# Optimization experiments

Measured on AMD Instinct MI355X. Metric: run time of the kernel, lower is better.

The kernel has to match this reference:

```python
import math
import jax, jax.numpy as jnp
import numpy as np

T, D, H, HD, ETA, R = 4096, 1024, 8, 64, 4, 7
EPS = 1e-5


def _discounted_sum(start_state, x, discounts):
    """state[t] = state[t-1]*discounts[t] + x[t], scanned over leading axis T."""
    def step(s, xd):
        xt, dt = xd
        s = s * dt + xt
        return s, s
    _, ys = jax.lax.scan(step, start_state, (x, discounts))
    return ys  # (T, *)


def _forward(inputs, terminations, tilde_k_prev, tilde_v_prev, s_prev, tick,
             W_kqv, b_kqv, W_p, b_p, W_proj, b_proj):
    cur_seq = inputs.shape[0]
    term = terminations.astype(inputs.dtype)

    kqv = (inputs @ W_kqv + b_kqv).reshape(cur_seq, H, 5 * HD)
    keys, queries, values, beta, gammas = jnp.split(kqv, 5, axis=-1)  # each (T,H,HD)
    p = (inputs @ W_p + b_p).reshape(cur_seq, H, 3 * ETA)
    p1, p2, p3 = jnp.split(p, 3, axis=-1)  # each (T,H,ETA)

    # feature-map expansion: outer product over (eta, head_dim) -> flatten to eta*HD
    keys = jnp.einsum('chd,chn->chnd', jax.nn.relu(keys), jax.nn.relu(p1)).reshape(cur_seq, H, ETA * HD)
    queries = jnp.einsum('chd,chn->chnd', jax.nn.relu(queries), jax.nn.relu(p2)).reshape(cur_seq, H, ETA * HD)
    gammas = jnp.einsum('chd,chn->chnd', jax.nn.sigmoid(gammas), jax.nn.sigmoid(p3)).reshape(cur_seq, H, ETA * HD)
    beta = jax.nn.sigmoid(beta)  # (T,H,HD)

    ticks = tick.reshape(1, 1) + jnp.arange(1, cur_seq + 1, dtype=inputs.dtype).reshape(-1, 1)  # (T,1)->(T,R)
    omegas = jnp.linspace(-math.pi, math.pi, R).astype(inputs.dtype).reshape(1, -1)
    occil = jnp.cos(ticks * omegas)  # (T,R)

    values = values * beta
    values = values[:, None, :, :] * occil[:, :, None, None]  # (T,R,H,HD)
    keys = keys * gammas
    s = keys  # (T,H,ETA*HD)
    keys = keys[:, None, :, :] * occil[:, :, None, None]  # (T,R,H,ETA*HD)

    not_term = (1.0 - term).reshape(cur_seq, 1, 1)
    discount_gamma = (1.0 - gammas) * not_term  # (T,H,ETA*HD)
    discount_beta = (1.0 - beta) * not_term     # (T,H,HD)

    final_keys = _discounted_sum(tilde_k_prev, keys, discount_gamma[:, None])    # (T,R,H,ETA*HD)
    final_values = _discounted_sum(tilde_v_prev, values, discount_beta[:, None])  # (T,R,H,HD)
    final_s = _discounted_sum(s_prev, s, discount_gamma)                          # (T,H,ETA*HD)

    kdq = jnp.einsum('crhd,chd->crh', final_keys, queries)
    kv = jnp.einsum('crhd,crh->chd', final_values, kdq)  # sum over r
    norm = jnp.einsum('chd,chd->ch', final_s, queries)
    attn_out = kv / (2 * R * norm[..., None] + EPS)
    attn_out = attn_out.reshape(cur_seq, H * HD) @ W_proj + b_proj  # dropout p=0.0 is identity

    new_tick = tick + cur_seq
    return attn_out, final_keys[-1], final_values[-1], final_s[-1], new_tick


def setup_inputs() -> dict:
    key = jax.random.key(0)
    ks = jax.random.split(key, 5)
    return {
        'inputs': jax.random.normal(ks[0], (T, D), jnp.float32),
        'terminations': jax.random.randint(ks[1], (T,), 0, 2, jnp.int32),
        'tilde_k_prev': jnp.zeros((R, H, ETA * HD), jnp.float32),
        'tilde_v_prev': jnp.zeros((R, H, HD), jnp.float32),
        's_prev': jnp.zeros((H, ETA * HD), jnp.float32),
        'tick': jnp.ones((1,), jnp.float32),
        'W_kqv': jax.random.normal(ks[2], (D, H * HD * 5), jnp.float32) * 0.02,
        'b_kqv': jnp.zeros((H * HD * 5,), jnp.float32),
        'W_p': jax.random.normal(ks[3], (D, H * ETA * 3), jnp.float32) * 0.02,
        'b_p': jnp.zeros((H * ETA * 3,), jnp.float32),
        'W_proj': jax.random.normal(ks[4], (H * HD, D), jnp.float32) * 0.02,
        'b_proj': jnp.zeros((D,), jnp.float32),
    }


def reference(inputs, terminations, tilde_k_prev, tilde_v_prev, s_prev, tick,
              W_kqv, b_kqv, W_p, b_p, W_proj, b_proj):
    return _forward(inputs, terminations, tilde_k_prev, tilde_v_prev, s_prev, tick,
                    W_kqv, b_kqv, W_p, b_p, W_proj, b_proj)
```

## Files before the change

kernel.cpp:

```cpp
#include <hip/hip_runtime.h>
#include <hip/hip_bf16.h>
#include <math.h>

#define T_SEQ 4096
#define DIM   1024
#define NH    8
#define HDIM  64
#define ETA   4
#define NR    7
#define NKQVC 2688
#define CHUNK 16
#define NCHUNK 256

typedef __attribute__((ext_vector_type(8))) short bf16x8;
typedef __attribute__((ext_vector_type(4))) short short4v;
typedef __attribute__((ext_vector_type(4))) float f32x4;

#define KQVC_OFF    0ul
#define OCC_OFF     5505024ul
#define BTPROJ_OFF  5537792ul
#define ATTNBF_OFF  5799936ul
#define BIASC_OFF   6848512ul
#define ABF_OFF     6851328ul
#define BTCAT_OFF   8948480ul
#define YSUM_OFF    6851328ul

#define O_ATTN 0ul
#define O_FK   4194304ul
#define O_FV   4208640ul
#define O_FS   4212224ul
#define O_TICK 4214272ul

__device__ __forceinline__ float sigm(float x) { return 1.f / (1.f + __expf(-x)); }

__device__ __forceinline__ short f2bf(float f) {
  union { __hip_bfloat16 b; short s; } u;
  u.b = __float2bfloat16(f);
  return u.s;
}
__device__ __forceinline__ float bf2f(short s) {
  union { __hip_bfloat16 b; short s2; } u;
  u.s2 = s;
  return __bfloat162float(u.b);
}

__device__ __forceinline__ void gload16(const void* g, void* l) {
  __builtin_amdgcn_global_load_lds(
      (const __attribute__((address_space(1))) void*)g,
      (__attribute__((address_space(3))) void*)l, 16, 0, 0);
}

__global__ __launch_bounds__(256) void cast_f32_bf16(
    const float* __restrict__ x, short* __restrict__ y) {
  size_t i = (size_t)(blockIdx.x * 256 + threadIdx.x) * 4;
  float4 v = *(const float4*)(x + i);
  short4v o;
  o.x = f2bf(v.x); o.y = f2bf(v.y); o.z = f2bf(v.z); o.w = f2bf(v.w);
  *(short4v*)(y + i) = o;
}

__global__ __launch_bounds__(256) void transpose_cast(
    const float* __restrict__ W, short* __restrict__ Bt, int K, int N) {
  __shared__ float tile[32][33];
  int n0 = blockIdx.x * 32, k0 = blockIdx.y * 32;
  int tx = threadIdx.x, ty = threadIdx.y;
  for (int i = ty; i < 32; i += 8)
    tile[i][tx] = W[(size_t)(k0 + i) * N + n0 + tx];
  __syncthreads();
  for (int i = ty; i < 32; i += 8)
    Bt[(size_t)(n0 + i) * K + k0 + tx] = f2bf(tile[tx][i]);
}

__global__ __launch_bounds__(256) void concat_bias(
    const float* __restrict__ b_kqv, const float* __restrict__ b_p,
    float* __restrict__ bc) {
  int i = blockIdx.x * 256 + threadIdx.x;
  if (i >= NKQVC) return;
  bc[i] = (i < 2560) ? b_kqv[i] : (i < 2656 ? b_p[i - 2560] : 0.f);
}

template <int OUT_BF16>
__global__ __launch_bounds__(256) void gemm_bt_mfma(
    const short* __restrict__ A, const short* __restrict__ Bt,
    const float* __restrict__ bias, void* __restrict__ Cout,
    int M, int N, int K) {
  __shared__ __align__(16) short lds[16384];

  int nwg = gridDim.x;
  int cpx = nwg >> 3;
  int bid = blockIdx.x;
  int swz = (bid & 7) * cpx + (bid >> 3);
  int nbx = N >> 7;
  int bm0 = (swz / nbx) << 7;
  int bn0 = (swz % nbx) << 7;

  const int tid = threadIdx.x;
  const int w = tid >> 6, l = tid & 63;
  const int wm = w >> 1, wn = w & 1;
  const int fr = l & 15;
  const int fq = l >> 4;

  const int ca = w * 2;
  const short* Ag0 = A + (size_t)(bm0 + ca * 16 + (l >> 2)) * K + (l & 3) * 8;
  const short* Ag1 = Ag0 + (size_t)16 * K;
  const short* Bg0 = Bt + (size_t)(bn0 + ca * 16 + (l >> 2)) * K + (l & 3) * 8;
  const short* Bg1 = Bg0 + (size_t)16 * K;

  f32x4 acc[4][4];
#pragma unroll
  for (int mi = 0; mi < 4; ++mi)
#pragma unroll
    for (int ni = 0; ni < 4; ++ni)
#pragma unroll
      for (int r = 0; r < 4; ++r) acc[mi][ni][r] = 0.f;

  const int KT = K >> 5;
  int cur = 0;
  {
    short* la = &lds[ca * 512];
    short* lb = &lds[4096 + ca * 512];
    gload16(Ag0, la);
    gload16(Ag1, la + 512);
    gload16(Bg0, lb);
    gload16(Bg1, lb + 512);
  }
  __syncthreads();

  for (int kt = 0; kt < KT; ++kt) {
    if (kt + 1 < KT) {
      int nb = (cur ^ 1) * 8192;
      int ko = (kt + 1) * 32;
      short* la = &lds[nb + ca * 512];
      short* lb = &lds[nb + 4096 + ca * 512];
      gload16(Ag0 + ko, la);
      gload16(Ag1 + ko, la + 512);
      gload16(Bg0 + ko, lb);
      gload16(Bg1 + ko, lb + 512);
    }
    const short* ArP = &lds[cur * 8192 + (wm * 64 + fr) * 32 + fq * 8];
    const short* BrP = &lds[cur * 8192 + 4096 + (wn * 64 + fr) * 32 + fq * 8];
    bf16x8 af[4], bfv[4];
#pragma unroll
    for (int mi = 0; mi < 4; ++mi) af[mi] = *(const bf16x8*)(ArP + mi * 512);
#pragma unroll
    for (int ni = 0; ni < 4; ++ni) bfv[ni] = *(const bf16x8*)(BrP + ni * 512);
#pragma unroll
    for (int mi = 0; mi < 4; ++mi)
#pragma unroll
      for (int ni = 0; ni < 4; ++ni)
        acc[mi][ni] = __builtin_amdgcn_mfma_f32_16x16x32_bf16(
            af[mi], bfv[ni], acc[mi][ni], 0, 0, 0);
    __syncthreads();
    cur ^= 1;
  }

  if (OUT_BF16) {
#pragma unroll
    for (int ni = 0; ni < 4; ++ni) {
      int col = wn * 64 + ni * 16 + fr;
      float bz = bias[bn0 + col];
#pragma unroll
      for (int mi = 0; mi < 4; ++mi) {
        int row = wm * 64 + mi * 16 + fq * 4;
#pragma unroll
        for (int r = 0; r < 4; ++r)
          lds[(row + r) * 128 + col] = f2bf(acc[mi][ni][r] + bz);
      }
    }
    __syncthreads();
    int row = tid >> 1, half = tid & 1;
    const f32x4* src = (const f32x4*)&lds[row * 128 + half * 64];
    f32x4* dst = (f32x4*)((short*)Cout + (size_t)(bm0 + row) * N + bn0 + half * 64);
#pragma unroll
    for (int i = 0; i < 8; ++i) dst[i] = src[i];
  } else {
#pragma unroll
    for (int ni = 0; ni < 4; ++ni) {
      int col = bn0 + wn * 64 + ni * 16 + fr;
      float bz = bias[col];
#pragma unroll
      for (int mi = 0; mi < 4; ++mi) {
        int row = bm0 + wm * 64 + mi * 16 + fq * 4;
#pragma unroll
        for (int r = 0; r < 4; ++r)
          ((float*)Cout)[(size_t)(row + r) * N + col] = acc[mi][ni][r] + bz;
      }
    }
  }
}

__global__ __launch_bounds__(256) void occil_kernel(const float* __restrict__ tick,
                                                    float* __restrict__ occ) {
  int t = blockIdx.x * 256 + threadIdx.x;
  if (t >= T_SEQ) return;
  float tickt = tick[0] + (float)(t + 1);
#pragma unroll
  for (int r = 0; r < NR; ++r) {
    float om = (float)(-3.14159265358979323846 + r * (3.14159265358979323846 / 3.0));
    occ[t * 8 + r] = cosf(tickt * om);
  }
  occ[t * 8 + 7] = 0.f;
}

__global__ __launch_bounds__(64) void pass_a(
    const short* __restrict__ kqv, const float* __restrict__ occ,
    const int* __restrict__ term, float* __restrict__ ysum) {
  const int c = blockIdx.x, h = blockIdx.y, dd = threadIdx.x;
  __shared__ float sp[CHUNK][12];
  __shared__ float socc[CHUNK][8];
  __shared__ float snt[CHUNK];
  for (int i = dd; i < CHUNK * 12; i += 64) {
    int t = i / 12, j = i - t * 12;
    sp[t][j] = bf2f(kqv[(size_t)(c * CHUNK + t) * NKQVC + 2560 + h * 12 + j]);
  }
  for (int i = dd; i < CHUNK * 8; i += 64)
    socc[i >> 3][i & 7] = occ[(size_t)c * CHUNK * 8 + i];
  for (int t = dd; t < CHUNK; t += 64)
    snt[t] = 1.f - (float)term[c * CHUNK + t];
  __syncthreads();

  float yk[NR][ETA], yv[NR], ys[ETA], Pg[ETA], Pb = 1.f;
#pragma unroll
  for (int r = 0; r < NR; ++r) {
    yv[r] = 0.f;
#pragma unroll
    for (int n = 0; n < ETA; ++n) yk[r][n] = 0.f;
  }
#pragma unroll
  for (int n = 0; n < ETA; ++n) { ys[n] = 0.f; Pg[n] = 1.f; }

  size_t bcur = (size_t)(c * CHUNK) * NKQVC + h * 320 + dd;
  short ck = kqv[bcur], cv = kqv[bcur + 128], cbt = kqv[bcur + 192], cg = kqv[bcur + 256];
  for (int t = 0; t < CHUNK; ++t) {
    size_t bnx = bcur + (t < CHUNK - 1 ? NKQVC : 0);
    short nk = kqv[bnx], nv = kqv[bnx + 128], nbt = kqv[bnx + 192], ng = kqv[bnx + 256];

    float nt = snt[t];
    float rk = fmaxf(bf2f(ck), 0.f);
    float sg = sigm(bf2f(cg));
    float sb = sigm(bf2f(cbt));
    float occr[NR];
#pragma unroll
    for (int r = 0; r < NR; ++r) occr[r] = socc[t][r];
#pragma unroll
    for (int n = 0; n < ETA; ++n) {
      float rp1 = fmaxf(sp[t][n], 0.f);
      float sp3 = sigm(sp[t][8 + n]);
      float gam = sg * sp3;
      float xs  = rk * rp1 * gam;
      float dg  = (1.f - gam) * nt;
      Pg[n] *= dg;
      ys[n] = fmaf(ys[n], dg, xs);
#pragma unroll
      for (int r = 0; r < NR; ++r)
        yk[r][n] = fmaf(yk[r][n], dg, xs * occr[r]);
    }
    float vb = bf2f(cv) * sb;
    float db = (1.f - sb) * nt;
    Pb *= db;
#pragma unroll
    for (int r = 0; r < NR; ++r) yv[r] = fmaf(yv[r], db, vb * occr[r]);

    ck = nk; cv = nv; cbt = nbt; cg = ng; bcur = bnx;
  }

  float* o = ysum + (size_t)(c * NH + h) * 44 * 64 + dd;
#pragma unroll
  for (int r = 0; r < NR; ++r)
#pragma unroll
    for (int n = 0; n < ETA; ++n) o[(r * 4 + n) * 64] = yk[r][n];
#pragma unroll
  for (int r = 0; r < NR; ++r) o[(28 + r) * 64] = yv[r];
#pragma unroll
  for (int n = 0; n < ETA; ++n) o[(35 + n) * 64] = ys[n];
#pragma unroll
  for (int n = 0; n < ETA; ++n) o[(39 + n) * 64] = Pg[n];
  o[43 * 64] = Pb;
}

__global__ __launch_bounds__(256) void pass_b(
    float* __restrict__ ysum, const float* __restrict__ k_prev,
    const float* __restrict__ v_prev, const float* __restrict__ s_prev) {
  int idx = blockIdx.x * 256 + threadIdx.x;
  int dd = idx & 63;
  int slot = (idx >> 6) % 39;
  int h = idx / (39 * 64);

  int pslot;
  float f;
  if (slot < 28) {
    int r = slot >> 2, n = slot & 3;
    f = k_prev[(size_t)(r * NH + h) * 256 + n * 64 + dd];
    pslot = 39 + n;
  } else if (slot < 35) {
    int r = slot - 28;
    f = v_prev[(size_t)(r * NH + h) * 64 + dd];
    pslot = 43;
  } else {
    int n = slot - 35;
    f = s_prev[(size_t)h * 256 + n * 64 + dd];
    pslot = 39 + n;
  }
  const size_t STRIDE = (size_t)NH * 2816;
  float* yb = ysum + (size_t)h * 2816 + slot * 64 + dd;
  const float* pb = ysum + (size_t)h * 2816 + pslot * 64 + dd;

#define PD 16
  float yring[PD], pring[PD];
#pragma unroll
  for (int d = 0; d < PD; ++d) {
    yring[d] = yb[(size_t)d * STRIDE];
    pring[d] = pb[(size_t)d * STRIDE];
  }
  const int NB = NCHUNK / PD;
  for (int cb = 0; cb < NB; ++cb) {
    int c0 = cb * PD;
    float ynext[PD], pnext[PD];
    if (cb + 1 < NB) {
#pragma unroll
      for (int j = 0; j < PD; ++j) {
        ynext[j] = yb[(size_t)(c0 + PD + j) * STRIDE];
        pnext[j] = pb[(size_t)(c0 + PD + j) * STRIDE];
      }
    }
#pragma unroll
    for (int j = 0; j < PD; ++j) {
      yb[(size_t)(c0 + j) * STRIDE] = f;
      f = fmaf(f, pring[j], yring[j]);
    }
    if (cb + 1 < NB) {
#pragma unroll
      for (int j = 0; j < PD; ++j) { yring[j] = ynext[j]; pring[j] = pnext[j]; }
    }
  }
#undef PD
}

__global__ __launch_bounds__(64) void pass_c(
    const short* __restrict__ kqv, const float* __restrict__ occ,
    const int* __restrict__ term, const float* __restrict__ carry,
    short* __restrict__ attn, float* __restrict__ out,
    const float* __restrict__ tick) {
  const int c = blockIdx.x, h = blockIdx.y, dd = threadIdx.x;
  __shared__ float sp[CHUNK][12];
  __shared__ float socc[CHUNK][8];
  __shared__ float snt[CHUNK];
  for (int i = dd; i < CHUNK * 12; i += 64) {
    int t = i / 12, j = i - t * 12;
    sp[t][j] = bf2f(kqv[(size_t)(c * CHUNK + t) * NKQVC + 2560 + h * 12 + j]);
  }
  for (int i = dd; i < CHUNK * 8; i += 64)
    socc[i >> 3][i & 7] = occ[(size_t)c * CHUNK * 8 + i];
  for (int t = dd; t < CHUNK; t += 64)
    snt[t] = 1.f - (float)term[c * CHUNK + t];

  const float* cp = carry + (size_t)(c * NH + h) * 2816 + dd;
  float fk[NR][ETA], fv[NR], fs[ETA];
#pragma unroll
  for (int r = 0; r < NR; ++r) {
#pragma unroll
    for (int n = 0; n < ETA; ++n) fk[r][n] = cp[(r * 4 + n) * 64];
    fv[r] = cp[(28 + r) * 64];
  }
#pragma unroll
  for (int n = 0; n < ETA; ++n) fs[n] = cp[(35 + n) * 64];
  __syncthreads();

  size_t bcur = (size_t)(c * CHUNK) * NKQVC + h * 320 + dd;
  short ck = kqv[bcur], cq = kqv[bcur + 64], cv = kqv[bcur + 128],
        cbt = kqv[bcur + 192], cg = kqv[bcur + 256];
  for (int t = 0; t < CHUNK; ++t) {
    size_t bnx = bcur + (t < CHUNK - 1 ? NKQVC : 0);
    short nk = kqv[bnx], nq = kqv[bnx + 64], nv = kqv[bnx + 128],
          nbt = kqv[bnx + 192], ng = kqv[bnx + 256];

    float nt = snt[t];
    float rk = fmaxf(bf2f(ck), 0.f);
    float rq = fmaxf(bf2f(cq), 0.f);
    float sg = sigm(bf2f(cg));
    float sb = sigm(bf2f(cbt));
    float occr[NR];
#pragma unroll
    for (int r = 0; r < NR; ++r) occr[r] = socc[t][r];
    float kdqp[NR];
#pragma unroll
    for (int r = 0; r < NR; ++r) kdqp[r] = 0.f;
    float normp = 0.f;
#pragma unroll
    for (int n = 0; n < ETA; ++n) {
      float rp1 = fmaxf(sp[t][n], 0.f);
      float rp2 = fmaxf(sp[t][4 + n], 0.f);
      float sp3 = sigm(sp[t][8 + n]);
      float gam = sg * sp3;
      float xs  = rk * rp1 * gam;
      float dg  = (1.f - gam) * nt;
      float qf  = rq * rp2;
      fs[n] = fmaf(fs[n], dg, xs);
      normp = fmaf(fs[n], qf, normp);
#pragma unroll
      for (int r = 0; r < NR; ++r) {
        fk[r][n] = fmaf(fk[r][n], dg, xs * occr[r]);
        kdqp[r]  = fmaf(fk[r][n], qf, kdqp[r]);
      }
    }
    float vb = bf2f(cv) * sb;
    float db = (1.f - sb) * nt;
#pragma unroll
    for (int r = 0; r < NR; ++r) fv[r] = fmaf(fv[r], db, vb * occr[r]);

    float red[8];
#pragma unroll
    for (int r = 0; r < NR; ++r) red[r] = kdqp[r];
    red[7] = normp;
#pragma unroll
    for (int i = 0; i < 8; ++i) {
      float x = red[i];
#pragma unroll
      for (int m = 1; m < 64; m <<= 1) x += __shfl_xor(x, m, 64);
      red[i] = x;
    }
    float denom = fmaf(14.f, red[7], 1e-5f);
    float kvv = 0.f;
#pragma unroll
    for (int r = 0; r < NR; ++r) kvv = fmaf(fv[r], red[r], kvv);
    attn[(size_t)(c * CHUNK + t) * 512 + h * 64 + dd] = f2bf(kvv / denom);

    ck = nk; cq = nq; cv = nv; cbt = nbt; cg = ng; bcur = bnx;
  }

  if (c == NCHUNK - 1) {
#pragma unroll
    for (int r = 0; r < NR; ++r) {
#pragma unroll
      for (int n = 0; n < ETA; ++n)
        out[O_FK + (size_t)(r * NH + h) * 256 + n * 64 + dd] = fk[r][n];
      out[O_FV + (size_t)(r * NH + h) * 64 + dd] = fv[r];
    }
#pragma unroll
    for (int n = 0; n < ETA; ++n)
      out[O_FS + (size_t)h * 256 + n * 64 + dd] = fs[n];
    if (h == 0 && dd == 0) out[O_TICK] = tick[0] + (float)T_SEQ;
  }
}

extern "C" void kernel_launch(void* const* d_in, const int* in_sizes, int n_in,
                              void* d_out, int out_size, void* d_ws, size_t ws_size,
                              hipStream_t stream) {
  const float* inputs = (const float*)d_in[0];
  const int*   term   = (const int*)d_in[1];
  const float* k_prev = (const float*)d_in[2];
  const float* v_prev = (const float*)d_in[3];
  const float* s_prev = (const float*)d_in[4];
  const float* tick   = (const float*)d_in[5];
  const float* W_kqv  = (const float*)d_in[6];
  const float* b_kqv  = (const float*)d_in[7];
  const float* W_p    = (const float*)d_in[8];
  const float* b_p    = (const float*)d_in[9];
  const float* W_proj = (const float*)d_in[10];
  const float* b_proj = (const float*)d_in[11];
  float* out = (float*)d_out;
  float* ws  = (float*)d_ws;

  short* kqvc   = (short*)(ws + KQVC_OFF);
  float* occ    = ws + OCC_OFF;
  short* BtProj = (short*)(ws + BTPROJ_OFF);
  short* attnbf = (short*)(ws + ATTNBF_OFF);
  float* biasc  = ws + BIASC_OFF;
  short* Abf    = (short*)(ws + ABF_OFF);
  short* BtCat  = (short*)(ws + BTCAT_OFF);
  float* ysum   = ws + YSUM_OFF;

  cast_f32_bf16<<<4096, 256, 0, stream>>>(inputs, Abf);
  transpose_cast<<<dim3(80, 32), dim3(32, 8), 0, stream>>>(W_kqv, BtCat, 1024, 2560);
  transpose_cast<<<dim3(3, 32), dim3(32, 8), 0, stream>>>(
      W_p, BtCat + (size_t)2560 * 1024, 1024, 96);
  transpose_cast<<<dim3(32, 16), dim3(32, 8), 0, stream>>>(W_proj, BtProj, 512, 1024);
  concat_bias<<<11, 256, 0, stream>>>(b_kqv, b_p, biasc);

  occil_kernel<<<16, 256, 0, stream>>>(tick, occ);

  gemm_bt_mfma<1><<<672, 256, 0, stream>>>(Abf, BtCat, biasc, kqvc,
                                           T_SEQ, NKQVC, DIM);

  pass_a<<<dim3(NCHUNK, NH), 64, 0, stream>>>(kqvc, occ, term, ysum);
  pass_b<<<78, 256, 0, stream>>>(ysum, k_prev, v_prev, s_prev);
  pass_c<<<dim3(NCHUNK, NH), 64, 0, stream>>>(kqvc, occ, term, ysum,
                                              attnbf, out, tick);

  gemm_bt_mfma<0><<<256, 256, 0, stream>>>(attnbf, BtProj, b_proj, out,
                                           T_SEQ, DIM, NH * HDIM);
}
```

Baseline: 143.0 us.

## Split oscillator frequencies across two wavefronts in chunked scan passes

pass_a and pass_c now launch two wavefronts per (chunk, head) block. One wave handles frequencies 0-3 and the other handles 4-6 plus the s-state. In pass_c, partial attention numerators and the denominator are exchanged through double-buffered shared memory with a per-timestep barrier. The aim is to halve per-thread serial work and register pressure and to double the number of waves available to hide latency. The cost is a __syncthreads every timestep, some duplicated gate computation, and idle lanes because the work splits 4 to 3.

```diff
diff --git a/kernel.cpp b/kernel.cpp
--- a/kernel.cpp
+++ b/kernel.cpp
@@ -202,29 +202,33 @@
   occ[t * 8 + 7] = 0.f;
 }
 
-__global__ __launch_bounds__(64) void pass_a(
+__global__ __launch_bounds__(128) void pass_a(
     const short* __restrict__ kqv, const float* __restrict__ occ,
     const int* __restrict__ term, float* __restrict__ ysum) {
-  const int c = blockIdx.x, h = blockIdx.y, dd = threadIdx.x;
+  const int c = blockIdx.x, h = blockIdx.y;
+  const int tid = threadIdx.x;
+  const int w = tid >> 6, dd = tid & 63;
+  const int R0 = w ? 4 : 0;
+  const int RN = w ? 3 : 4;
   __shared__ float sp[CHUNK][12];
   __shared__ float socc[CHUNK][8];
   __shared__ float snt[CHUNK];
-  for (int i = dd; i < CHUNK * 12; i += 64) {
+  for (int i = tid; i < CHUNK * 12; i += 128) {
     int t = i / 12, j = i - t * 12;
     sp[t][j] = bf2f(kqv[(size_t)(c * CHUNK + t) * NKQVC + 2560 + h * 12 + j]);
   }
-  for (int i = dd; i < CHUNK * 8; i += 64)
+  for (int i = tid; i < CHUNK * 8; i += 128)
     socc[i >> 3][i & 7] = occ[(size_t)c * CHUNK * 8 + i];
-  for (int t = dd; t < CHUNK; t += 64)
+  for (int t = tid; t < CHUNK; t += 128)
     snt[t] = 1.f - (float)term[c * CHUNK + t];
   __syncthreads();
 
-  float yk[NR][ETA], yv[NR], ys[ETA], Pg[ETA], Pb = 1.f;
-#pragma unroll
-  for (int r = 0; r < NR; ++r) {
-    yv[r] = 0.f;
-#pragma unroll
-    for (int n = 0; n < ETA; ++n) yk[r][n] = 0.f;
+  float yk[4][ETA], yv[4], ys[ETA], Pg[ETA], Pb = 1.f;
+#pragma unroll
+  for (int rr = 0; rr < 4; ++rr) {
+    yv[rr] = 0.f;
+#pragma unroll
+    for (int n = 0; n < ETA; ++n) yk[rr][n] = 0.f;
   }
 #pragma unroll
   for (int n = 0; n < ETA; ++n) { ys[n] = 0.f; Pg[n] = 1.f; }
@@ -239,9 +243,9 @@
     float rk = fmaxf(bf2f(ck), 0.f);
     float sg = sigm(bf2f(cg));
     float sb = sigm(bf2f(cbt));
-    float occr[NR];
-#pragma unroll
-    for (int r = 0; r < NR; ++r) occr[r] = socc[t][r];
+    float occr[4];
+#pragma unroll
+    for (int rr = 0; rr < 4; ++rr) occr[rr] = socc[t][R0 + rr];
 #pragma unroll
     for (int n = 0; n < ETA; ++n) {
       float rp1 = fmaxf(sp[t][n], 0.f);
@@ -249,33 +253,40 @@
       float gam = sg * sp3;
       float xs  = rk * rp1 * gam;
       float dg  = (1.f - gam) * nt;
-      Pg[n] *= dg;
-      ys[n] = fmaf(ys[n], dg, xs);
-#pragma unroll
-      for (int r = 0; r < NR; ++r)
-        yk[r][n] = fmaf(yk[r][n], dg, xs * occr[r]);
+      if (w) {
+        Pg[n] *= dg;
+        ys[n] = fmaf(ys[n], dg, xs);
+      }
+#pragma unroll
+      for (int rr = 0; rr < 4; ++rr)
+        if (rr < RN) yk[rr][n] = fmaf(yk[rr][n], dg, xs * occr[rr]);
     }
     float vb = bf2f(cv) * sb;
     float db = (1.f - sb) * nt;
-    Pb *= db;
-#pragma unroll
-    for (int r = 0; r < NR; ++r) yv[r] = fmaf(yv[r], db, vb * occr[r]);
+    if (!w) Pb *= db;
+#pragma unroll
+    for (int rr = 0; rr < 4; ++rr)
+      if (rr < RN) yv[rr] = fmaf(yv[rr], db, vb * occr[rr]);
 
     ck = nk; cv = nv; cbt = nbt; cg = ng; bcur = bnx;
   }
 
   float* o = ysum + (size_t)(c * NH + h) * 44 * 64 + dd;
 #pragma unroll
-  for (int r = 0; r < NR; ++r)
-#pragma unroll
-    for (int n = 0; n < ETA; ++n) o[(r * 4 + n) * 64] = yk[r][n];
-#pragma unroll
-  for (int r = 0; r < NR; ++r) o[(28 + r) * 64] = yv[r];
-#pragma unroll
-  for (int n = 0; n < ETA; ++n) o[(35 + n) * 64] = ys[n];
-#pragma unroll
-  for (int n = 0; n < ETA; ++n) o[(39 + n) * 64] = Pg[n];
-  o[43 * 64] = Pb;
+  for (int rr = 0; rr < 4; ++rr)
+    if (rr < RN) {
+#pragma unroll
+      for (int n = 0; n < ETA; ++n) o[((R0 + rr) * 4 + n) * 64] = yk[rr][n];
+      o[(28 + R0 + rr) * 64] = yv[rr];
+    }
+  if (w) {
+#pragma unroll
+    for (int n = 0; n < ETA; ++n) o[(35 + n) * 64] = ys[n];
+#pragma unroll
+    for (int n = 0; n < ETA; ++n) o[(39 + n) * 64] = Pg[n];
+  } else {
+    o[43 * 64] = Pb;
+  }
 }
 
 __global__ __launch_bounds__(256) void pass_b(
@@ -336,34 +347,42 @@
 #undef PD
 }
 
-__global__ __launch_bounds__(64) void pass_c(
+__global__ __launch_bounds__(128) void pass_c(
     const short* __restrict__ kqv, const float* __restrict__ occ,
     const int* __restrict__ term, const float* __restrict__ carry,
     short* __restrict__ attn, float* __restrict__ out,
     const float* __restrict__ tick) {
-  const int c = blockIdx.x, h = blockIdx.y, dd = threadIdx.x;
+  const int c = blockIdx.x, h = blockIdx.y;
+  const int tid = threadIdx.x;
+  const int w = tid >> 6, dd = tid & 63;
+  const int R0 = w ? 4 : 0;
+  const int RN = w ? 3 : 4;
   __shared__ float sp[CHUNK][12];
   __shared__ float socc[CHUNK][8];
   __shared__ float snt[CHUNK];
-  for (int i = dd; i < CHUNK * 12; i += 64) {
+  __shared__ float xch[2][2][64];
+  for (int i = tid; i < CHUNK * 12; i += 128) {
     int t = i / 12, j = i - t * 12;
     sp[t][j] = bf2f(kqv[(size_t)(c * CHUNK + t) * NKQVC + 2560 + h * 12 + j]);
   }
-  for (int i = dd; i < CHUNK * 8; i += 64)
+  for (int i = tid; i < CHUNK * 8; i += 128)
     socc[i >> 3][i & 7] = occ[(size_t)c * CHUNK * 8 + i];
-  for (int t = dd; t < CHUNK; t += 64)
+  for (int t = tid; t < CHUNK; t += 128)
     snt[t] = 1.f - (float)term[c * CHUNK + t];
 
   const float* cp = carry + (size_t)(c * NH + h) * 2816 + dd;
-  float fk[NR][ETA], fv[NR], fs[ETA];
-#pragma unroll
-  for (int r = 0; r < NR; ++r) {
-#pragma unroll
-    for (int n = 0; n < ETA; ++n) fk[r][n] = cp[(r * 4 + n) * 64];
-    fv[r] = cp[(28 + r) * 64];
-  }
-#pragma unroll
-  for (int n = 0; n < ETA; ++n) fs[n] = cp[(35 + n) * 64];
+  float fk[4][ETA], fv[4], fs[ETA];
+#pragma unroll
+  for (int rr = 0; rr < 4; ++rr)
+    if (rr < RN) {
+#pragma unroll
+      for (int n = 0; n < ETA; ++n) fk[rr][n] = cp[((R0 + rr) * 4 + n) * 64];
+      fv[rr] = cp[(28 + R0 + rr) * 64];
+    }
+  if (w) {
+#pragma unroll
+    for (int n = 0; n < ETA; ++n) fs[n] = cp[(35 + n) * 64];
+  }
   __syncthreads();
 
   size_t bcur = (size_t)(c * CHUNK) * NKQVC + h * 320 + dd;
@@ -379,12 +398,10 @@
     float rq = fmaxf(bf2f(cq), 0.f);
     float sg = sigm(bf2f(cg));
     float sb = sigm(bf2f(cbt));
-    float occr[NR];
-#pragma unroll
-    for (int r = 0; r < NR; ++r) occr[r] = socc[t][r];
-    float kdqp[NR];
-#pragma unroll
-    for (int r = 0; r < NR; ++r) kdqp[r] = 0.f;
+    float occr[4];
+#pragma unroll
+    for (int rr = 0; rr < 4; ++rr) occr[rr] = socc[t][R0 + rr];
+    float kdqp[4] = {0.f, 0.f, 0.f, 0.f};
     float normp = 0.f;
 #pragma unroll
     for (int n = 0; n < ETA; ++n) {
@@ -395,51 +412,70 @@
       float xs  = rk * rp1 * gam;
       float dg  = (1.f - gam) * nt;
       float qf  = rq * rp2;
-      fs[n] = fmaf(fs[n], dg, xs);
-      normp = fmaf(fs[n], qf, normp);
-#pragma unroll
-      for (int r = 0; r < NR; ++r) {
-        fk[r][n] = fmaf(fk[r][n], dg, xs * occr[r]);
-        kdqp[r]  = fmaf(fk[r][n], qf, kdqp[r]);
+      if (w) {
+        fs[n] = fmaf(fs[n], dg, xs);
+        normp = fmaf(fs[n], qf, normp);
       }
+#pragma unroll
+      for (int rr = 0; rr < 4; ++rr)
+        if (rr < RN) {
+          fk[rr][n] = fmaf(fk[rr][n], dg, xs * occr[rr]);
+          kdqp[rr]  = fmaf(fk[rr][n], qf, kdqp[rr]);
+        }
     }
     float vb = bf2f(cv) * sb;
     float db = (1.f - sb) * nt;
 #pragma unroll
-    for (int r = 0; r < NR; ++r) fv[r] = fmaf(fv[r], db, vb * occr[r]);
-
-    float red[8];
-#pragma unroll
-    for (int r = 0; r < NR; ++r) red[r] = kdqp[r];
-    red[7] = normp;
-#pragma unroll
-    for (int i = 0; i < 8; ++i) {
+    for (int rr = 0; rr < 4; ++rr)
+      if (rr < RN) fv[rr] = fmaf(fv[rr], db, vb * occr[rr]);
+
+    float red[4];
+    red[0] = kdqp[0]; red[1] = kdqp[1]; red[2] = kdqp[2];
+    red[3] = w ? normp : kdqp[3];
+#pragma unroll
+    for (int i = 0; i < 4; ++i) {
       float x = red[i];
 #pragma unroll
       for (int m = 1; m < 64; m <<= 1) x += __shfl_xor(x, m, 64);
       red[i] = x;
     }
-    float denom = fmaf(14.f, red[7], 1e-5f);
-    float kvv = 0.f;
-#pragma unroll
-    for (int r = 0; r < NR; ++r) kvv = fmaf(fv[r], red[r], kvv);
-    attn[(size_t)(c * CHUNK + t) * 512 + h * 64 + dd] = f2bf(kvv / denom);
+    int par = t & 1;
+    if (w) {
+      float kvv1 = fv[0] * red[0];
+      kvv1 = fmaf(fv[1], red[1], kvv1);
+      kvv1 = fmaf(fv[2], red[2], kvv1);
+      float denom = fmaf(14.f, red[3], 1e-5f);
+      xch[par][0][dd] = kvv1;
+      xch[par][1][dd] = denom;
+    }
+    __syncthreads();
+    if (!w) {
+      float kvv = fv[0] * red[0];
+      kvv = fmaf(fv[1], red[1], kvv);
+      kvv = fmaf(fv[2], red[2], kvv);
+      kvv = fmaf(fv[3], red[3], kvv);
+      kvv += xch[par][0][dd];
+      attn[(size_t)(c * CHUNK + t) * 512 + h * 64 + dd] = f2bf(kvv / xch[par][1][dd]);
+    }
 
     ck = nk; cq = nq; cv = nv; cbt = nbt; cg = ng; bcur = bnx;
   }
 
   if (c == NCHUNK - 1) {
 #pragma unroll
-    for (int r = 0; r < NR; ++r) {
+    for (int rr = 0; rr < 4; ++rr)
+      if (rr < RN) {
+#pragma unroll
+        for (int n = 0; n < ETA; ++n)
+          out[O_FK + (size_t)((R0 + rr) * NH + h) * 256 + n * 64 + dd] = fk[rr][n];
+        out[O_FV + (size_t)((R0 + rr) * NH + h) * 64 + dd] = fv[rr];
+      }
+    if (w) {
 #pragma unroll
       for (int n = 0; n < ETA; ++n)
-        out[O_FK + (size_t)(r * NH + h) * 256 + n * 64 + dd] = fk[r][n];
-      out[O_FV + (size_t)(r * NH + h) * 64 + dd] = fv[r];
-    }
-#pragma unroll
-    for (int n = 0; n < ETA; ++n)
-      out[O_FS + (size_t)h * 256 + n * 64 + dd] = fs[n];
-    if (h == 0 && dd == 0) out[O_TICK] = tick[0] + (float)T_SEQ;
+        out[O_FS + (size_t)h * 256 + n * 64 + dd] = fs[n];
+    }
+    if (!w && h == 0 && dd == 0) out[O_TICK] = tick[0] + (float)T_SEQ;
   }
 }
 
@@ -482,10 +518,10 @@
   gemm_bt_mfma<1><<<672, 256, 0, stream>>>(Abf, BtCat, biasc, kqvc,
                                            T_SEQ, NKQVC, DIM);
 
-  pass_a<<<dim3(NCHUNK, NH), 64, 0, stream>>>(kqvc, occ, term, ysum);
+  pass_a<<<dim3(NCHUNK, NH), 128, 0, stream>>>(kqvc, occ, term, ysum);
   pass_b<<<78, 256, 0, stream>>>(ysum, k_prev, v_prev, s_prev);
-  pass_c<<<dim3(NCHUNK, NH), 64, 0, stream>>>(kqvc, occ, term, ysum,
-                                              attnbf, out, tick);
+  pass_c<<<dim3(NCHUNK, NH), 128, 0, stream>>>(kqvc, occ, term, ysum,
+                                               attnbf, out, tick);
 
   gemm_bt_mfma<0><<<256, 256, 0, stream>>>(attnbf, BtProj, b_proj, out,
                                            T_SEQ, DIM, NH * HDIM);
```

New measurement: 151.3 us. +5.8%, slower.
